# Kernel tuning notes

Measured on AMD Instinct MI355X. Metric: run time of the kernel, lower is better.

The kernel has to match this reference:

```python
import jax, jax.numpy as jnp
import numpy as np

D_MODEL = 1024
N_HEADS = 16
HEAD_DIM = D_MODEL // N_HEADS


def setup_inputs() -> dict:
    key = jax.random.key(0)
    k1, k2, k3 = jax.random.split(key, 3)
    x = jax.random.normal(k1, (2, 2048, D_MODEL), dtype=jnp.float32)
    w_qkv = jax.random.normal(k2, (3 * D_MODEL, D_MODEL), dtype=jnp.float32) * 0.02
    w_out = jax.random.normal(k3, (D_MODEL, D_MODEL), dtype=jnp.float32) * 0.02
    return {"x": x, "w_qkv": w_qkv, "w_out": w_out}


def reference(x, w_qkv, w_out):
    B, T, D = x.shape
    H, Hd = N_HEADS, HEAD_DIM
    # QKV projection: Linear stores weight as [out, in] -> '...i,oi->...o'
    qkv = jnp.einsum('bti,oi->bto', x, w_qkv)              # [B, T, 3D]
    # split (3*H, Hs) group-major, chunk into q/k/v of H heads each
    qkv = qkv.reshape(B, T, 3, H, Hd)
    q = jnp.transpose(qkv[:, :, 0], (0, 2, 1, 3))          # [B, H, T, Hd]
    k = jnp.transpose(qkv[:, :, 1], (0, 2, 1, 3))
    v = jnp.transpose(qkv[:, :, 2], (0, 2, 1, 3))
    scale = 1.0 / jnp.sqrt(jnp.asarray(Hd, dtype=x.dtype))
    scores = jnp.einsum('bhqd,bhkd->bhqk', q, k) * scale   # [B, H, T, T]
    causal = jnp.tril(jnp.ones((T, T), dtype=bool))        # [T, T]
    scores = jnp.where(causal[None, None], scores, jnp.asarray(-jnp.inf, dtype=scores.dtype))
    attn = jax.nn.softmax(scores, axis=-1)
    ctx = jnp.einsum('bhqk,bhkd->bhqd', attn, v)           # [B, H, T, Hd]
    ctx = jnp.transpose(ctx, (0, 2, 1, 3)).reshape(B, T, D)
    return jnp.einsum('bti,oi->bto', ctx, w_out)
```

## Files before the change

kernel.cpp:

```cpp
#include <hip/hip_runtime.h>


typedef short short8 __attribute__((ext_vector_type(8)));
typedef float f32x4 __attribute__((ext_vector_type(4)));
typedef unsigned short u16;
typedef unsigned int u32;

#define T_SEQ 2048
#define N_B 2
#define N_H 16
#define HD 64
#define DM 1024
#define TRIPLE 3072

__device__ __forceinline__ u16 f2bf(float f) {
  union { float f; unsigned u; } v;
  v.f = f;
  unsigned r = v.u + 0x7fffu + ((v.u >> 16) & 1u);
  return (u16)(r >> 16);
}

__device__ __forceinline__ float bf2f(u16 x) {
  return __uint_as_float((u32)x << 16);
}

__device__ __forceinline__ u32 cvtpk(float a, float b) {
  u32 r;
  asm("v_cvt_pk_bf16_f32 %0, %1, %2" : "=v"(r) : "v"(a), "v"(b));
  return r;
}

typedef const __attribute__((address_space(1))) void gvoid;
typedef __attribute__((address_space(3))) void lvoid;

__device__ __forceinline__ void g2l16(const void* g, void* l) {
  __builtin_amdgcn_global_load_lds((gvoid*)g, (lvoid*)l, 16, 0, 0);
}

__device__ __forceinline__ void storeC(float* p, float v) { *p = v; }
__device__ __forceinline__ void storeC(u16* p, float v) { *p = f2bf(v); }

__global__ __launch_bounds__(256) void cast_all(const float4* __restrict__ x,
                                                const float4* __restrict__ wq,
                                                const float4* __restrict__ wo,
                                                ushort4* __restrict__ out) {
  int i = blockIdx.x * 256 + threadIdx.x;
  const float4* src;
  int off;
  if (i < 1048576) { src = x; off = 0; }
  else if (i < 1835008) { src = wq; off = 1048576; }
  else { src = wo; off = 1835008; }
  float4 v = src[i - off];
  ushort4 o;
  o.x = f2bf(v.x); o.y = f2bf(v.y); o.z = f2bf(v.z); o.w = f2bf(v.w);
  out[i] = o;
}

__global__ __launch_bounds__(256) void vtrans(const u16* __restrict__ qkv,
                                              u16* __restrict__ vT) {
  const int tid = threadIdx.x;
  const int w = tid >> 6, lane = tid & 63;
  const int ti = lane >> 3, di = lane & 7;
  const int h = blockIdx.y, b = blockIdx.z;
  const int t0 = blockIdx.x * 256 + w * 64 + ti * 8;

  const u16* src = qkv + (size_t)(b * T_SEQ + t0) * TRIPLE + 2 * DM + h * HD + di * 8;
  u32 x[8][4];
#pragma unroll
  for (int e = 0; e < 8; ++e) {
    union { short8 v; u32 u[4]; } cv;
    cv.v = *(const short8*)(src + (size_t)e * TRIPLE);
#pragma unroll
    for (int j = 0; j < 4; ++j) x[e][j] = cv.u[j];
  }
  u32 y[8][4];
#pragma unroll
  for (int a = 0; a < 4; ++a)
#pragma unroll
    for (int j = 0; j < 4; ++j) {
      u32 lo = x[2 * a][j], hi = x[2 * a + 1][j];
      y[2 * a][j] = (lo & 0x0000FFFFu) | (hi << 16);
      y[2 * a + 1][j] = (lo >> 16) | (hi & 0xFFFF0000u);
    }
  u16* dst = vT + ((size_t)(b * N_H + h) * HD + di * 8) * T_SEQ + t0;
#pragma unroll
  for (int dd = 0; dd < 8; ++dd) {
    union { short8 v; u32 u[4]; } cv;
#pragma unroll
    for (int a = 0; a < 4; ++a) cv.u[a] = y[2 * a + (dd & 1)][dd >> 1];
    *(short8*)(dst + (size_t)dd * T_SEQ) = cv.v;
  }
}

template <typename OutT>
__global__ __launch_bounds__(256) void gemm_bt(const u16* __restrict__ A,
                                               const u16* __restrict__ W,
                                               OutT* __restrict__ C,
                                               int M, int N, int K) {
  __shared__ char As[128 * 64 * 2];
  __shared__ char Bs[128 * 64 * 2];
  const int tid = threadIdx.x;
  const int lane = tid & 63, w = tid >> 6;
  const int l15 = lane & 15, l4 = lane >> 4;
  const int m0 = blockIdx.y * 128, n0 = blockIdx.x * 128;
  const int wr = (w >> 1) * 64, wc = (w & 1) * 64;

  const f32x4 zero = {0.f, 0.f, 0.f, 0.f};
  f32x4 acc[4][4];
#pragma unroll
  for (int m = 0; m < 4; ++m)
#pragma unroll
    for (int n = 0; n < 4; ++n) acc[m][n] = zero;

  for (int k0 = 0; k0 < K; k0 += 64) {
#pragma unroll
    for (int i = 0; i < 4; ++i) {
      const int cb = (i * 4 + w) * 64;
      const int c = cb + lane;
      const int row = c >> 3;
      const int ks = ((c & 7) ^ (row & 7)) * 8;
      g2l16(A + (size_t)(m0 + row) * K + k0 + ks, As + (size_t)cb * 16);
      g2l16(W + (size_t)(n0 + row) * K + k0 + ks, Bs + (size_t)cb * 16);
    }
    __syncthreads();

#pragma unroll
    for (int kk = 0; kk < 2; ++kk) {
      short8 a[4], b[4];
#pragma unroll
      for (int m = 0; m < 4; ++m) {
        int row = wr + m * 16 + l15;
        int slot = (kk * 4 + l4) ^ (row & 7);
        a[m] = *(const short8*)(As + row * 128 + slot * 16);
      }
#pragma unroll
      for (int n = 0; n < 4; ++n) {
        int row = wc + n * 16 + l15;
        int slot = (kk * 4 + l4) ^ (row & 7);
        b[n] = *(const short8*)(Bs + row * 128 + slot * 16);
      }
#pragma unroll
      for (int m = 0; m < 4; ++m)
#pragma unroll
        for (int n = 0; n < 4; ++n)
          acc[m][n] = __builtin_amdgcn_mfma_f32_16x16x32_bf16(a[m], b[n], acc[m][n], 0, 0, 0);
    }
    __syncthreads();
  }

#pragma unroll
  for (int m = 0; m < 4; ++m)
#pragma unroll
    for (int n = 0; n < 4; ++n)
#pragma unroll
      for (int r = 0; r < 4; ++r) {
        int row = m0 + wr + m * 16 + l4 * 4 + r;
        int col = n0 + wc + n * 16 + l15;
        storeC(C + (size_t)row * N + col, acc[m][n][r]);
      }
}

__global__ __launch_bounds__(256) void attn_fwd(const u16* __restrict__ qkv,
                                                const u16* __restrict__ vT,
                                                u16* __restrict__ ctx) {
  __shared__ char Ks[2][8192];
  __shared__ char Vs[2][8192];
  __shared__ char Pl[4][2048];

  const int tid = threadIdx.x;
  const int lane = tid & 63, w = tid >> 6;
  const int l15 = lane & 15, l4 = lane >> 4;
  const int h = blockIdx.y, b = blockIdx.z;
  const int g = h + N_H * b;
  const int qt = (blockIdx.x + 9 * g) & 31;
  const int q0 = qt * 64;
  const int qrow = q0 + w * 16 + l15;
  const int ktmax = qt;

  const float c_log2 = 0.18033688011112042f;
  short8 qa[2];
  {
    const u16* qp = qkv + (size_t)(b * T_SEQ + q0 + w * 16 + l15) * TRIPLE + h * HD;
#pragma unroll
    for (int kk = 0; kk < 2; ++kk) {
      short8 raw = *(const short8*)(qp + kk * 32 + l4 * 8);
      union { short8 v; u32 w4[4]; } qq;
#pragma unroll
      for (int j = 0; j < 4; ++j)
        qq.w4[j] = cvtpk(bf2f((u16)raw[2 * j]) * c_log2,
                         bf2f((u16)raw[2 * j + 1]) * c_log2);
      qa[kk] = qq.v;
    }
  }

  const int r0 = tid >> 3, c0 = tid & 7;
  const u16* kptr0 = qkv + (size_t)(b * T_SEQ + r0) * TRIPLE + DM + h * HD +
                     ((c0 ^ (r0 & 7)) << 3);
  const u16* kptr1 = kptr0 + (size_t)32 * TRIPLE;
  const u16* vptr0 = vT + ((size_t)g * HD + r0) * T_SEQ + ((c0 ^ (r0 & 7)) << 3);
  const u16* vptr1 = vptr0 + (size_t)32 * T_SEQ;

  char* Plb = Pl[w];

  const f32x4 zero = {0.f, 0.f, 0.f, 0.f};
  f32x4 o[4];
#pragma unroll
  for (int nt = 0; nt < 4; ++nt) o[nt] = zero;
  float mr = -INFINITY, lr = 0.f;

  g2l16(kptr0, Ks[0] + tid * 16);
  g2l16(kptr1, Ks[0] + (256 + tid) * 16);
  g2l16(vptr0, Vs[0] + tid * 16);
  g2l16(vptr1, Vs[0] + (256 + tid) * 16);
  kptr0 += (size_t)64 * TRIPLE; kptr1 += (size_t)64 * TRIPLE;
  vptr0 += 64; vptr1 += 64;
  __syncthreads();

  for (int kt = 0;; ++kt) {
    const int cur = kt & 1;
    const int k0 = kt * 64;

    if (kt < ktmax) {
      g2l16(kptr0, Ks[cur ^ 1] + tid * 16);
      g2l16(kptr1, Ks[cur ^ 1] + (256 + tid) * 16);
      g2l16(vptr0, Vs[cur ^ 1] + tid * 16);
      g2l16(vptr1, Vs[cur ^ 1] + (256 + tid) * 16);
      kptr0 += (size_t)64 * TRIPLE; kptr1 += (size_t)64 * TRIPLE;
      vptr0 += 64; vptr1 += 64;
    }

    f32x4 s[4];
#pragma unroll
    for (int mt = 0; mt < 4; ++mt) s[mt] = zero;
#pragma unroll
    for (int kk = 0; kk < 2; ++kk) {
#pragma unroll
      for (int mt = 0; mt < 4; ++mt) {
        int row = mt * 16 + l15;
        int slot = (kk * 4 + l4) ^ (row & 7);
        short8 kb = *(const short8*)(Ks[cur] + row * 128 + slot * 16);
        s[mt] = __builtin_amdgcn_mfma_f32_16x16x32_bf16(kb, qa[kk], s[mt], 0, 0, 0);
      }
    }

    if (kt == ktmax) {
#pragma unroll
      for (int mt = 0; mt < 4; ++mt)
#pragma unroll
        for (int r = 0; r < 4; ++r) {
          int key = k0 + mt * 16 + l4 * 4 + r;
          if (key > qrow) s[mt][r] = -INFINITY;
        }
    }

    float mx = fmaxf(fmaxf(fmaxf(s[0][0], s[0][1]), fmaxf(s[0][2], s[0][3])),
                     fmaxf(fmaxf(s[1][0], s[1][1]), fmaxf(s[1][2], s[1][3])));
    mx = fmaxf(mx, fmaxf(fmaxf(fmaxf(s[2][0], s[2][1]), fmaxf(s[2][2], s[2][3])),
                         fmaxf(fmaxf(s[3][0], s[3][1]), fmaxf(s[3][2], s[3][3]))));
    mx = fmaxf(mx, __shfl_xor(mx, 16));
    mx = fmaxf(mx, __shfl_xor(mx, 32));
    if (!__all(mx - mr <= 8.0f)) {
      float mn = fmaxf(mr, mx);
      float fr = exp2f(mr - mn);
      lr *= fr;
#pragma unroll
      for (int r = 0; r < 4; ++r) {
        float frq = __shfl(fr, l4 * 4 + r);
#pragma unroll
        for (int nt = 0; nt < 4; ++nt) o[nt][r] *= frq;
      }
      mr = mn;
    }
    float ps = 0.f;
#pragma unroll
    for (int mt = 0; mt < 4; ++mt)
#pragma unroll
      for (int r = 0; r < 4; ++r) {
        float p = exp2f(s[mt][r] - mr);
        s[mt][r] = p;
        ps += p;
      }
    lr += ps;

#pragma unroll
    for (int mt = 0; mt < 4; ++mt) {
      uint2 pw;
      pw.x = cvtpk(s[mt][0], s[mt][1]);
      pw.y = cvtpk(s[mt][2], s[mt][3]);
      int slot = ((mt * 2 + (l4 >> 1)) ^ (l15 & 7));
      *(uint2*)(Plb + l15 * 128 + (slot << 4) + ((l4 & 1) << 3)) = pw;
    }

#pragma unroll
    for (int kk = 0; kk < 2; ++kk) {
      short8 pa = *(const short8*)(Plb + l15 * 128 + (((kk * 4 + l4) ^ (l15 & 7)) << 4));
#pragma unroll
      for (int nt = 0; nt < 4; ++nt) {
        int d = nt * 16 + l15;
        int slot = (kk * 4 + l4) ^ (l15 & 7);
        short8 vb = *(const short8*)(Vs[cur] + d * 128 + slot * 16);
        o[nt] = __builtin_amdgcn_mfma_f32_16x16x32_bf16(pa, vb, o[nt], 0, 0, 0);
      }
    }

    if (kt == ktmax) break;
    __syncthreads();
  }

  lr += __shfl_xor(lr, 16);
  lr += __shfl_xor(lr, 32);
#pragma unroll
  for (int r = 0; r < 4; ++r) {
    float lrq = __shfl(lr, l4 * 4 + r);
    float inv = __builtin_amdgcn_rcpf(lrq);
    size_t t = (size_t)(b * T_SEQ + q0 + w * 16 + l4 * 4 + r);
#pragma unroll
    for (int nt = 0; nt < 4; ++nt)
      ctx[t * DM + h * HD + nt * 16 + l15] = f2bf(o[nt][r] * inv);
  }
}

extern "C" void kernel_launch(void* const* d_in, const int* in_sizes, int n_in,
                              void* d_out, int out_size, void* d_ws, size_t ws_size,
                              hipStream_t stream) {
  const float* x = (const float*)d_in[0];
  const float* wqkv = (const float*)d_in[1];
  const float* wout = (const float*)d_in[2];
  float* out = (float*)d_out;
  char* ws = (char*)d_ws;

  u16* xb    = (u16*)(ws);
  u16* wqkvb = (u16*)(ws + 8u * 1024 * 1024);
  u16* woutb = (u16*)(ws + 14u * 1024 * 1024);
  u16* qkvb  = (u16*)(ws + 16u * 1024 * 1024);
  u16* ctxb  = (u16*)(ws + 40u * 1024 * 1024);
  u16* vTb   = (u16*)(ws + 48u * 1024 * 1024);

  cast_all<<<8192, 256, 0, stream>>>((const float4*)x, (const float4*)wqkv,
                                     (const float4*)wout, (ushort4*)xb);

  gemm_bt<u16><<<dim3(24, 32), 256, 0, stream>>>(xb, wqkvb, qkvb, 4096, 3072, 1024);

  vtrans<<<dim3(8, N_H, N_B), 256, 0, stream>>>(qkvb, vTb);

  attn_fwd<<<dim3(32, N_H, N_B), 256, 0, stream>>>(qkvb, vTb, ctxb);

  gemm_bt<float><<<dim3(8, 32), 256, 0, stream>>>(ctxb, woutb, out, 4096, 1024, 1024);
}
```

Measured before the change: 135.5 us.

## Pair short and long causal query tiles per block for balanced attention work

The attention kernel now uses 128-thread blocks, each handling two 32-row query tiles (p and 63-p), processed back to back, so every block does roughly equal causal work. K/V staging is rewritten as a macro that loads a full 64-key tile with 128 threads, and the pipeline restarts at key tile 0 when switching passes. This removes tail imbalance from causal triangles, at the cost of fewer warps per block, reloading K/V for the second pass, and wasted masked work on 64-key diagonal tiles for 32-row queries.

Measured after the change: 148.8 us. +9.8%, slower.

```diff
diff --git a/kernel.cpp b/kernel.cpp
--- a/kernel.cpp
+++ b/kernel.cpp
@@ -160,27 +160,28 @@
       }
 }
 
-__global__ __launch_bounds__(256) void attn_fwd(const u16* __restrict__ qkv,
+__global__ __launch_bounds__(128) void attn_fwd(const u16* __restrict__ qkv,
                                                 const u16* __restrict__ vT,
                                                 u16* __restrict__ ctx) {
   __shared__ char Ks[2][8192];
   __shared__ char Vs[2][8192];
-  __shared__ char Pl[4][2048];
+  __shared__ char Pl[2][2048];
 
   const int tid = threadIdx.x;
   const int lane = tid & 63, w = tid >> 6;
   const int l15 = lane & 15, l4 = lane >> 4;
   const int h = blockIdx.y, b = blockIdx.z;
   const int g = h + N_H * b;
-  const int qt = (blockIdx.x + 9 * g) & 31;
-  const int q0 = qt * 64;
-  const int qrow = q0 + w * 16 + l15;
-  const int ktmax = qt;
+  const int p = blockIdx.x;
+  const int qtile[2] = {p, 63 - p};
+  const int nA = ((32 * p + 31) >> 6) + 1;
+  const int nTot = nA + ((2047 - 32 * p) >> 6) + 1;
 
   const float c_log2 = 0.18033688011112042f;
-  short8 qa[2];
-  {
-    const u16* qp = qkv + (size_t)(b * T_SEQ + q0 + w * 16 + l15) * TRIPLE + h * HD;
+  short8 qa2[2][2];
+#pragma unroll
+  for (int ps = 0; ps < 2; ++ps) {
+    const u16* qp = qkv + (size_t)(b * T_SEQ + 32 * qtile[ps] + w * 16 + l15) * TRIPLE + h * HD;
 #pragma unroll
     for (int kk = 0; kk < 2; ++kk) {
       short8 raw = *(const short8*)(qp + kk * 32 + l4 * 8);
@@ -189,16 +190,25 @@
       for (int j = 0; j < 4; ++j)
         qq.w4[j] = cvtpk(bf2f((u16)raw[2 * j]) * c_log2,
                          bf2f((u16)raw[2 * j + 1]) * c_log2);
-      qa[kk] = qq.v;
+      qa2[ps][kk] = qq.v;
     }
   }
 
   const int r0 = tid >> 3, c0 = tid & 7;
-  const u16* kptr0 = qkv + (size_t)(b * T_SEQ + r0) * TRIPLE + DM + h * HD +
-                     ((c0 ^ (r0 & 7)) << 3);
-  const u16* kptr1 = kptr0 + (size_t)32 * TRIPLE;
-  const u16* vptr0 = vT + ((size_t)g * HD + r0) * T_SEQ + ((c0 ^ (r0 & 7)) << 3);
-  const u16* vptr1 = vptr0 + (size_t)32 * T_SEQ;
+  const int swz = (c0 ^ (r0 & 7)) << 3;
+  const u16* kbase = qkv + (size_t)(b * T_SEQ + r0) * TRIPLE + DM + h * HD + swz;
+  const u16* vbase = vT + ((size_t)g * HD + r0) * T_SEQ + swz;
+
+#define STAGE(kt_, buf_)                                                        \
+  {                                                                             \
+    const int kb_ = (kt_) * 64;                                                 \
+    _Pragma("unroll") for (int i_ = 0; i_ < 4; ++i_) {                          \
+      g2l16(kbase + (size_t)(kb_ + 16 * i_) * TRIPLE,                           \
+            Ks[buf_] + tid * 16 + i_ * 2048);                                   \
+      g2l16(vbase + (size_t)(16 * i_) * T_SEQ + kb_,                            \
+            Vs[buf_] + tid * 16 + i_ * 2048);                                   \
+    }                                                                           \
+  }
 
   char* Plb = Pl[w];
 
@@ -208,47 +218,45 @@
   for (int nt = 0; nt < 4; ++nt) o[nt] = zero;
   float mr = -INFINITY, lr = 0.f;
 
-  g2l16(kptr0, Ks[0] + tid * 16);
-  g2l16(kptr1, Ks[0] + (256 + tid) * 16);
-  g2l16(vptr0, Vs[0] + tid * 16);
-  g2l16(vptr1, Vs[0] + (256 + tid) * 16);
-  kptr0 += (size_t)64 * TRIPLE; kptr1 += (size_t)64 * TRIPLE;
-  vptr0 += 64; vptr1 += 64;
+  int pass = 0;
+  int q0 = 32 * qtile[0];
+  int ktm = nA - 1;
+  short8 qa0 = qa2[0][0], qa1 = qa2[0][1];
+
+  STAGE(0, 0);
   __syncthreads();
-
-  for (int kt = 0;; ++kt) {
-    const int cur = kt & 1;
-    const int k0 = kt * 64;
-
-    if (kt < ktmax) {
-      g2l16(kptr0, Ks[cur ^ 1] + tid * 16);
-      g2l16(kptr1, Ks[cur ^ 1] + (256 + tid) * 16);
-      g2l16(vptr0, Vs[cur ^ 1] + tid * 16);
-      g2l16(vptr1, Vs[cur ^ 1] + (256 + tid) * 16);
-      kptr0 += (size_t)64 * TRIPLE; kptr1 += (size_t)64 * TRIPLE;
-      vptr0 += 64; vptr1 += 64;
+  int cur = 0;
+
+  for (int i = 0;; ++i) {
+    const int kt = pass ? i - nA : i;
+    const bool diag = (kt == ktm);
+
+    if (i + 1 < nTot) {
+      const int nkt = diag ? 0 : kt + 1;
+      STAGE(nkt, cur ^ 1);
     }
 
     f32x4 s[4];
 #pragma unroll
     for (int mt = 0; mt < 4; ++mt) s[mt] = zero;
 #pragma unroll
-    for (int kk = 0; kk < 2; ++kk) {
-#pragma unroll
-      for (int mt = 0; mt < 4; ++mt) {
-        int row = mt * 16 + l15;
-        int slot = (kk * 4 + l4) ^ (row & 7);
-        short8 kb = *(const short8*)(Ks[cur] + row * 128 + slot * 16);
-        s[mt] = __builtin_amdgcn_mfma_f32_16x16x32_bf16(kb, qa[kk], s[mt], 0, 0, 0);
-      }
-    }
-
-    if (kt == ktmax) {
+    for (int mt = 0; mt < 4; ++mt) {
+      int row = mt * 16 + l15;
+      int slot0 = l4 ^ (row & 7);
+      short8 kb0 = *(const short8*)(Ks[cur] + row * 128 + slot0 * 16);
+      s[mt] = __builtin_amdgcn_mfma_f32_16x16x32_bf16(kb0, qa0, s[mt], 0, 0, 0);
+      int slot1 = (4 + l4) ^ (row & 7);
+      short8 kb1 = *(const short8*)(Ks[cur] + row * 128 + slot1 * 16);
+      s[mt] = __builtin_amdgcn_mfma_f32_16x16x32_bf16(kb1, qa1, s[mt], 0, 0, 0);
+    }
+
+    if (diag) {
+      const int qrow = q0 + w * 16 + l15;
 #pragma unroll
       for (int mt = 0; mt < 4; ++mt)
 #pragma unroll
         for (int r = 0; r < 4; ++r) {
-          int key = k0 + mt * 16 + l4 * 4 + r;
+          int key = kt * 64 + mt * 16 + l4 * 4 + r;
           if (key > qrow) s[mt][r] = -INFINITY;
         }
     }
@@ -276,9 +284,9 @@
     for (int mt = 0; mt < 4; ++mt)
 #pragma unroll
       for (int r = 0; r < 4; ++r) {
-        float p = exp2f(s[mt][r] - mr);
-        s[mt][r] = p;
-        ps += p;
+        float pv = exp2f(s[mt][r] - mr);
+        s[mt][r] = pv;
+        ps += pv;
       }
     lr += ps;
 
@@ -303,21 +311,32 @@
       }
     }
 
-    if (kt == ktmax) break;
+    if (diag) {
+      lr += __shfl_xor(lr, 16);
+      lr += __shfl_xor(lr, 32);
+#pragma unroll
+      for (int r = 0; r < 4; ++r) {
+        float lrq = __shfl(lr, l4 * 4 + r);
+        float inv = __builtin_amdgcn_rcpf(lrq);
+        size_t t = (size_t)(b * T_SEQ + q0 + w * 16 + l4 * 4 + r);
+#pragma unroll
+        for (int nt = 0; nt < 4; ++nt)
+          ctx[t * DM + h * HD + nt * 16 + l15] = f2bf(o[nt][r] * inv);
+      }
+      if (pass == 1) break;
+      pass = 1;
+      q0 = 32 * qtile[1];
+      ktm = nTot - nA - 1;
+      qa0 = qa2[1][0]; qa1 = qa2[1][1];
+#pragma unroll
+      for (int nt = 0; nt < 4; ++nt) o[nt] = zero;
+      mr = -INFINITY; lr = 0.f;
+    }
+
     __syncthreads();
-  }
-
-  lr += __shfl_xor(lr, 16);
-  lr += __shfl_xor(lr, 32);
-#pragma unroll
-  for (int r = 0; r < 4; ++r) {
-    float lrq = __shfl(lr, l4 * 4 + r);
-    float inv = __builtin_amdgcn_rcpf(lrq);
-    size_t t = (size_t)(b * T_SEQ + q0 + w * 16 + l4 * 4 + r);
-#pragma unroll
-    for (int nt = 0; nt < 4; ++nt)
-      ctx[t * DM + h * HD + nt * 16 + l15] = f2bf(o[nt][r] * inv);
-  }
+    cur ^= 1;
+  }
+#undef STAGE
 }
 
 extern "C" void kernel_launch(void* const* d_in, const int* in_sizes, int n_in,
@@ -343,7 +362,7 @@
 
   vtrans<<<dim3(8, N_H, N_B), 256, 0, stream>>>(qkvb, vTb);
 
-  attn_fwd<<<dim3(32, N_H, N_B), 256, 0, stream>>>(qkvb, vTb, ctxb);
+  attn_fwd<<<dim3(32, N_H, N_B), 128, 0, stream>>>(qkvb, vTb, ctxb);
 
   gemm_bt<float><<<dim3(8, 32), 256, 0, stream>>>(ctxb, woutb, out, 4096, 1024, 1024);
 }
```
